# Performance work log

Hardware: AMD Instinct MI355X
Metric: run time of the kernel (lower is better)

## Reference

```python
import jax, jax.numpy as jnp
import numpy as np

N, P, D = 262144, 128, 64
EPS = 1e-5
NEG = -1e30


def setup_inputs() -> dict:
    key = jax.random.key(0)
    ks = jax.random.split(key, 12)
    feature = jax.random.normal(ks[0], (N, D), jnp.float32)
    feature_geo = jax.random.normal(ks[1], (N, D), jnp.float32)
    xyz = jax.random.uniform(ks[2], (N, 3), jnp.float32)
    centers = jax.random.uniform(ks[3], (3,), jnp.float32)
    plane_center = jax.random.uniform(ks[4], (P, 3), jnp.float32)
    nrm = jax.random.normal(ks[5], (P, 3), jnp.float32)
    plane_normal = nrm / jnp.linalg.norm(nrm, axis=1, keepdims=True)
    lo = 0.3 * jax.random.uniform(ks[6], (P, 3), jnp.float32)
    hi = 0.5 + 0.5 * jax.random.uniform(ks[7], (P, 3), jnp.float32)
    # exactly two active axes per plane (one axis of the aabb is zeroed)
    ax = jnp.arange(P) % 3
    keep = (jnp.arange(3)[None, :] != ax[:, None]).astype(jnp.float32)
    plane_xyz_min = lo * keep
    plane_xyz_max = hi * keep
    w1 = 0.05 * jax.random.normal(ks[8], (2 * D, D), jnp.float32)
    b1 = jnp.zeros((D,), jnp.float32)
    w2 = 0.05 * jax.random.normal(ks[9], (D, D), jnp.float32)
    b2 = jnp.zeros((D,), jnp.float32)
    w3 = 0.05 * jax.random.normal(ks[10], (D, 1), jnp.float32)
    b3 = jnp.zeros((1,), jnp.float32)
    g1 = jnp.ones((D,), jnp.float32); be1 = jnp.zeros((D,), jnp.float32)
    m1 = jnp.zeros((D,), jnp.float32); v1 = jnp.ones((D,), jnp.float32)
    g2 = jnp.ones((D,), jnp.float32); be2 = jnp.zeros((D,), jnp.float32)
    m2 = jnp.zeros((D,), jnp.float32); v2 = jnp.ones((D,), jnp.float32)
    return dict(feature=feature, feature_geo=feature_geo, xyz=xyz, centers=centers,
                plane_center=plane_center, plane_normal=plane_normal,
                plane_xyz_min=plane_xyz_min, plane_xyz_max=plane_xyz_max,
                w1=w1, b1=b1, g1=g1, be1=be1, m1=m1, v1=v1,
                w2=w2, b2=b2, g2=g2, be2=be2, m2=m2, v2=v2,
                w3=w3, b3=b3)


def _bn(x, g, b, m, v):
    return (x - m) * (g * jax.lax.rsqrt(v + EPS)) + b


def reference(feature, feature_geo, xyz, centers, plane_center, plane_normal,
              plane_xyz_min, plane_xyz_max, w1, b1, g1, be1, m1, v1,
              w2, b2, g2, be2, m2, v2, w3, b3):
    clouds = xyz + centers                                   # [N,3]
    f = jnp.concatenate([feature, feature_geo], axis=1)      # [N,2D]
    # 1x1 conv MLP == per-point matmul (fc1 -> fc2 with BN+ReLU, fc3)
    h1 = jax.nn.relu(_bn(f @ w1 + b1, g1, be1, m1, v1))      # [N,D]
    h2 = jax.nn.relu(_bn(h1 @ w2 + b2, g2, be2, m2, v2))     # [N,D]
    scores = jax.nn.relu(h2 @ w3 + b3)[:, 0]                 # [N]
    # per-plane aabb mask over the two active axes (xyz_max != 0)
    active = plane_xyz_max != 0                              # [P,3]
    in_rng = (clouds[None] >= plane_xyz_min[:, None]) & (clouds[None] < plane_xyz_max[:, None])
    range_mask = jnp.all(in_rng | ~active[:, None, :], axis=-1)   # [P,N]
    # point-to-plane distance: |(clouds - center) . normal|
    dots = clouds @ plane_normal.T                           # [N,P]
    offs = jnp.sum(plane_center * plane_normal, axis=1)      # [P]
    dist = jnp.abs(dots - offs[None, :]).T                   # [P,N]
    mask = range_mask & (dist < 0.1)                         # [P,N]
    sig = jax.nn.sigmoid(scores)                             # [N]
    on_mask = mask & (sig > 0.5)[None, :]
    off_mask = mask & (sig <= 0.5)[None, :]

    def pool(m):  # masked max-pool of fc2 features over points of one plane
        val = jnp.max(jnp.where(m[:, None], h2, NEG), axis=0)     # [D]
        return jnp.where(jnp.any(m), val, 0.0)

    on_feat = jax.lax.map(pool, on_mask)                     # [P,D]
    off_feat = jax.lax.map(pool, off_mask)                   # [P,D]
    scores_masked = jnp.where(mask, scores[None, :], 0.0)    # [P,N]
    return scores_masked, mask, on_mask, off_mask, on_feat, off_feat
```

## Files before the change

### kernel.cpp

```cpp
#include <hip/hip_runtime.h>
#include <hip/hip_bf16.h>
#include <math.h>

#define NPTS 262144
#define NP   128
#define DD   64
#define NWORDS (NPTS / 64)

__global__ __launch_bounds__(256) void mlp1_kernel(
    const float* __restrict__ feature, const float* __restrict__ feature_geo,
    const float* __restrict__ w1, const float* __restrict__ b1,
    const float* __restrict__ g1, const float* __restrict__ be1,
    const float* __restrict__ m1, const float* __restrict__ v1,
    float* __restrict__ h1_out)
{
    const int n = blockIdx.x * 256 + threadIdx.x;
    float acc[DD];
#pragma unroll
    for (int j = 0; j < DD; ++j) acc[j] = 0.0f;

    const float4* fA = reinterpret_cast<const float4*>(feature) + (size_t)n * 16;
#pragma unroll 1
    for (int q = 0; q < 16; ++q) {
        const float4 fv = fA[q];
        const float* wr = w1 + q * 4 * DD;
#pragma unroll
        for (int j = 0; j < DD; ++j) acc[j] = fmaf(fv.x, wr[j], acc[j]);
#pragma unroll
        for (int j = 0; j < DD; ++j) acc[j] = fmaf(fv.y, wr[DD + j], acc[j]);
#pragma unroll
        for (int j = 0; j < DD; ++j) acc[j] = fmaf(fv.z, wr[2 * DD + j], acc[j]);
#pragma unroll
        for (int j = 0; j < DD; ++j) acc[j] = fmaf(fv.w, wr[3 * DD + j], acc[j]);
    }
    const float4* fB = reinterpret_cast<const float4*>(feature_geo) + (size_t)n * 16;
    const float* w1b = w1 + DD * DD;
#pragma unroll 1
    for (int q = 0; q < 16; ++q) {
        const float4 fv = fB[q];
        const float* wr = w1b + q * 4 * DD;
#pragma unroll
        for (int j = 0; j < DD; ++j) acc[j] = fmaf(fv.x, wr[j], acc[j]);
#pragma unroll
        for (int j = 0; j < DD; ++j) acc[j] = fmaf(fv.y, wr[DD + j], acc[j]);
#pragma unroll
        for (int j = 0; j < DD; ++j) acc[j] = fmaf(fv.z, wr[2 * DD + j], acc[j]);
#pragma unroll
        for (int j = 0; j < DD; ++j) acc[j] = fmaf(fv.w, wr[3 * DD + j], acc[j]);
    }
#pragma unroll
    for (int j = 0; j < DD; ++j) {
        float sc = g1[j] * (1.0f / sqrtf(v1[j] + 1e-5f));
        float h  = fmaf(acc[j] + b1[j] - m1[j], sc, be1[j]);
        acc[j] = fmaxf(h, 0.0f);
    }
    float4* o = reinterpret_cast<float4*>(h1_out) + (size_t)n * 16;
#pragma unroll
    for (int q = 0; q < 16; ++q)
        o[q] = make_float4(acc[4*q+0], acc[4*q+1], acc[4*q+2], acc[4*q+3]);
}

__global__ __launch_bounds__(256) void mlp2_kernel(
    const float* __restrict__ h1_in,
    const float* __restrict__ w2, const float* __restrict__ b2,
    const float* __restrict__ g2, const float* __restrict__ be2,
    const float* __restrict__ m2, const float* __restrict__ v2,
    const float* __restrict__ w3, const float* __restrict__ b3,
    float* __restrict__ h2_out, float* __restrict__ scores_out)
{
    const int n = blockIdx.x * 256 + threadIdx.x;
    float acc[DD];
#pragma unroll
    for (int j = 0; j < DD; ++j) acc[j] = 0.0f;

    const float4* fA = reinterpret_cast<const float4*>(h1_in) + (size_t)n * 16;
#pragma unroll 1
    for (int q = 0; q < 16; ++q) {
        const float4 fv = fA[q];
        const float* wr = w2 + q * 4 * DD;
#pragma unroll
        for (int j = 0; j < DD; ++j) acc[j] = fmaf(fv.x, wr[j], acc[j]);
#pragma unroll
        for (int j = 0; j < DD; ++j) acc[j] = fmaf(fv.y, wr[DD + j], acc[j]);
#pragma unroll
        for (int j = 0; j < DD; ++j) acc[j] = fmaf(fv.z, wr[2 * DD + j], acc[j]);
#pragma unroll
        for (int j = 0; j < DD; ++j) acc[j] = fmaf(fv.w, wr[3 * DD + j], acc[j]);
    }
    float s = 0.0f;
#pragma unroll
    for (int j = 0; j < DD; ++j) {
        float sc = g2[j] * (1.0f / sqrtf(v2[j] + 1e-5f));
        float h  = fmaf(acc[j] + b2[j] - m2[j], sc, be2[j]);
        h = fmaxf(h, 0.0f);
        acc[j] = h;
        s = fmaf(h, w3[j], s);
    }
    s += b3[0];
    float4* o = reinterpret_cast<float4*>(h2_out) + (size_t)n * 16;
#pragma unroll
    for (int q = 0; q < 16; ++q)
        o[q] = make_float4(acc[4*q+0], acc[4*q+1], acc[4*q+2], acc[4*q+3]);
    scores_out[n] = fmaxf(s, 0.0f);
}

__global__ __launch_bounds__(256) void mask_kernel(
    const float* __restrict__ xyz, const float* __restrict__ centers,
    const float* __restrict__ plane_center, const float* __restrict__ plane_normal,
    const float* __restrict__ pmin, const float* __restrict__ pmax,
    const float* __restrict__ scores,
    float* __restrict__ out_sm, float* __restrict__ out_mask,
    float* __restrict__ out_on, float* __restrict__ out_off,
    unsigned long long* __restrict__ hitOn, unsigned long long* __restrict__ hitOff)
{
    __shared__ float4 pl[NP][3];
    const int t = threadIdx.x;
    if (t < NP) {
        float n0 = plane_normal[t*3+0], n1 = plane_normal[t*3+1], n2 = plane_normal[t*3+2];
        float c0 = plane_center[t*3+0], c1 = plane_center[t*3+1], c2 = plane_center[t*3+2];
        float off = (c0*n0 + c1*n1) + c2*n2;
        pl[t][0] = make_float4(n0, n1, n2, off);
        pl[t][1] = make_float4(pmin[t*3+0], pmin[t*3+1], pmin[t*3+2], 0.0f);
        pl[t][2] = make_float4(pmax[t*3+0], pmax[t*3+1], pmax[t*3+2], 0.0f);
    }
    __syncthreads();

    const int n = blockIdx.x * 256 + t;
    const float c0 = xyz[n*3+0] + centers[0];
    const float c1 = xyz[n*3+1] + centers[1];
    const float c2 = xyz[n*3+2] + centers[2];
    const float s  = scores[n];
    const bool on  = (0.5f + 0.5f * tanhf(0.5f * s)) > 0.5f;
    const int lane = t & 63;
    const int word = n >> 6;

    for (int p = 0; p < NP; ++p) {
        float4 nrm = pl[p][0];
        float4 mn  = pl[p][1];
        float4 mx  = pl[p][2];
        float d = fabsf(fmaf(c2, nrm.z, fmaf(c1, nrm.y, c0 * nrm.x)) - nrm.w);
        bool ok0 = (mx.x == 0.0f) | ((c0 >= mn.x) & (c0 < mx.x));
        bool ok1 = (mx.y == 0.0f) | ((c1 >= mn.y) & (c1 < mx.y));
        bool ok2 = (mx.z == 0.0f) | ((c2 >= mn.z) & (c2 < mx.z));
        bool mk  = ok0 & ok1 & ok2 & (d < 0.1f);
        size_t idx = (size_t)p * NPTS + n;
        out_sm[idx]   = mk ? s : 0.0f;
        out_mask[idx] = mk ? 1.0f : 0.0f;
        bool mon  = mk & on;
        bool moff = mk & (!on);
        out_on[idx]  = mon  ? 1.0f : 0.0f;
        out_off[idx] = moff ? 1.0f : 0.0f;
        unsigned long long bOn  = __ballot(mon);
        unsigned long long bOff = __ballot(moff);
        if (lane == 0) {
            hitOn [(size_t)p * NWORDS + word] = bOn;
            hitOff[(size_t)p * NWORDS + word] = bOff;
        }
    }
}

__global__ __launch_bounds__(256) void pool_kernel(
    const float* __restrict__ h2,
    const unsigned long long* __restrict__ hitOn,
    const unsigned long long* __restrict__ hitOff,
    float* __restrict__ partials)
{
    __shared__ float tile[128 * DD];
    __shared__ unsigned long long bm[2][NP][2];
    const int t = threadIdx.x;
    const int lane = t & 63;
    const int wv = t >> 6;

    float accOn[32], accOff[32];
#pragma unroll
    for (int i = 0; i < 32; ++i) { accOn[i] = 0.0f; accOff[i] = 0.0f; }

    for (int cc = 0; cc < 4; ++cc) {
        const int chunk = blockIdx.x * 4 + cc;
        const int base  = chunk * 128;
        const float4* src = reinterpret_cast<const float4*>(h2 + (size_t)base * DD);
        float4* dst = reinterpret_cast<float4*>(tile);
#pragma unroll
        for (int q = 0; q < 8; ++q) dst[t + q * 256] = src[t + q * 256];
        {
            const int p = t & 127;
            const int half = t >> 7;
            const unsigned long long* hsrc = half ? hitOff : hitOn;
            const int w0 = chunk * 2;
            bm[half][p][0] = hsrc[(size_t)p * NWORDS + w0 + 0];
            bm[half][p][1] = hsrc[(size_t)p * NWORDS + w0 + 1];
        }
        __syncthreads();

#pragma unroll
        for (int i = 0; i < 32; ++i) {
            const int p = wv * 32 + i;
            unsigned long long m;
            m = bm[0][p][0];
            while (m) { int nn = __builtin_ctzll(m); m &= m - 1;
                        accOn[i]  = fmaxf(accOn[i],  tile[nn * DD + lane]); }
            m = bm[0][p][1];
            while (m) { int nn = __builtin_ctzll(m); m &= m - 1;
                        accOn[i]  = fmaxf(accOn[i],  tile[(64 + nn) * DD + lane]); }
            m = bm[1][p][0];
            while (m) { int nn = __builtin_ctzll(m); m &= m - 1;
                        accOff[i] = fmaxf(accOff[i], tile[nn * DD + lane]); }
            m = bm[1][p][1];
            while (m) { int nn = __builtin_ctzll(m); m &= m - 1;
                        accOff[i] = fmaxf(accOff[i], tile[(64 + nn) * DD + lane]); }
        }
        __syncthreads();
    }
    const size_t bbase = (size_t)blockIdx.x * NP * 2 * DD;
#pragma unroll
    for (int i = 0; i < 32; ++i) {
        const int p = wv * 32 + i;
        partials[bbase + ((size_t)p * 2 + 0) * DD + lane] = accOn[i];
        partials[bbase + ((size_t)p * 2 + 1) * DD + lane] = accOff[i];
    }
}

__global__ __launch_bounds__(256) void reduce_kernel(
    const float* __restrict__ partials, float* __restrict__ out_feats)
{
    const int u = blockIdx.x * 256 + threadIdx.x;
    float a0 = 0.0f, a1 = 0.0f, a2 = 0.0f, a3 = 0.0f;
    for (int b = 0; b < 512; b += 4) {
        a0 = fmaxf(a0, partials[(size_t)(b + 0) * 16384 + u]);
        a1 = fmaxf(a1, partials[(size_t)(b + 1) * 16384 + u]);
        a2 = fmaxf(a2, partials[(size_t)(b + 2) * 16384 + u]);
        a3 = fmaxf(a3, partials[(size_t)(b + 3) * 16384 + u]);
    }
    const float acc = fmaxf(fmaxf(a0, a1), fmaxf(a2, a3));
    const int p = u >> 7, oo = (u >> 6) & 1, d = u & 63;
    out_feats[oo * (NP * DD) + p * DD + d] = acc;
}

extern "C" void kernel_launch(void* const* d_in, const int* in_sizes, int n_in,
                              void* d_out, int out_size, void* d_ws, size_t ws_size,
                              hipStream_t stream) {
    const float* feature      = (const float*)d_in[0];
    const float* feature_geo  = (const float*)d_in[1];
    const float* xyz          = (const float*)d_in[2];
    const float* centers      = (const float*)d_in[3];
    const float* plane_center = (const float*)d_in[4];
    const float* plane_normal = (const float*)d_in[5];
    const float* pmin         = (const float*)d_in[6];
    const float* pmax         = (const float*)d_in[7];
    const float* w1 = (const float*)d_in[8];
    const float* b1 = (const float*)d_in[9];
    const float* g1 = (const float*)d_in[10];
    const float* be1 = (const float*)d_in[11];
    const float* m1 = (const float*)d_in[12];
    const float* v1 = (const float*)d_in[13];
    const float* w2 = (const float*)d_in[14];
    const float* b2 = (const float*)d_in[15];
    const float* g2 = (const float*)d_in[16];
    const float* be2 = (const float*)d_in[17];
    const float* m2 = (const float*)d_in[18];
    const float* v2 = (const float*)d_in[19];
    const float* w3 = (const float*)d_in[20];
    const float* b3 = (const float*)d_in[21];

    float* out = (float*)d_out;
    const size_t PN = (size_t)NP * NPTS;
    float* out_sm    = out;
    float* out_mask  = out + PN;
    float* out_on    = out + 2 * PN;
    float* out_off   = out + 3 * PN;
    float* out_feats = out + 4 * PN;

    float* h1     = (float*)d_ws;
    float* h2     = h1 + (size_t)NPTS * DD;
    float* scores = h2 + (size_t)NPTS * DD;
    unsigned long long* hitOn  = (unsigned long long*)(scores + NPTS);
    unsigned long long* hitOff = hitOn + (size_t)NP * NWORDS;
    float* partials = h1;

    mlp1_kernel<<<NPTS / 256, 256, 0, stream>>>(
        feature, feature_geo, w1, b1, g1, be1, m1, v1, h1);
    mlp2_kernel<<<NPTS / 256, 256, 0, stream>>>(
        h1, w2, b2, g2, be2, m2, v2, w3, b3, h2, scores);
    mask_kernel<<<NPTS / 256, 256, 0, stream>>>(
        xyz, centers, plane_center, plane_normal, pmin, pmax, scores,
        out_sm, out_mask, out_on, out_off, hitOn, hitOff);
    pool_kernel<<<512, 256, 0, stream>>>(h2, hitOn, hitOff, partials);
    reduce_kernel<<<16384 / 256, 256, 0, stream>>>(partials, out_feats);
}
```

Measured before the change: 892.6 us.

## Replace partials reduction with atomicMax and precompute plane params in prep kernel

The per-block partials buffer and the separate reduce kernel are dropped. Each pool block now merges its nonzero results into the zero-initialised output with integer atomicMax on the float bits, which is valid because the values are non-negative after ReLU. A small prep kernel zeroes the output and packs the plane parameters once. The mask kernel then reads that packed data straight from global memory instead of rebuilding a shared-memory copy in every block. This removes a large partials write and read plus one launch, at the cost of atomic contention and uncached-in-LDS plane loads inside the mask loop.

```diff
diff --git a/kernel.cpp b/kernel.cpp
--- a/kernel.cpp
+++ b/kernel.cpp
@@ -6,6 +6,24 @@
 #define NP   128
 #define DD   64
 #define NWORDS (NPTS / 64)
+
+__global__ __launch_bounds__(256) void prep_kernel(
+    const float* __restrict__ plane_center, const float* __restrict__ plane_normal,
+    const float* __restrict__ pmin, const float* __restrict__ pmax,
+    float* __restrict__ packed, float* __restrict__ out_feats)
+{
+    const int t = threadIdx.x;
+    out_feats[blockIdx.x * 256 + t] = 0.0f;
+    if (blockIdx.x == 0 && t < NP) {
+        float n0 = plane_normal[t*3+0], n1 = plane_normal[t*3+1], n2 = plane_normal[t*3+2];
+        float c0 = plane_center[t*3+0], c1 = plane_center[t*3+1], c2 = plane_center[t*3+2];
+        float off = (c0*n0 + c1*n1) + c2*n2;
+        float4* pp = reinterpret_cast<float4*>(packed) + t * 3;
+        pp[0] = make_float4(n0, n1, n2, off);
+        pp[1] = make_float4(pmin[t*3+0], pmin[t*3+1], pmin[t*3+2], 0.0f);
+        pp[2] = make_float4(pmax[t*3+0], pmax[t*3+1], pmax[t*3+2], 0.0f);
+    }
+}
 
 __global__ __launch_bounds__(256) void mlp1_kernel(
     const float* __restrict__ feature, const float* __restrict__ feature_geo,
@@ -106,25 +124,13 @@
 
 __global__ __launch_bounds__(256) void mask_kernel(
     const float* __restrict__ xyz, const float* __restrict__ centers,
-    const float* __restrict__ plane_center, const float* __restrict__ plane_normal,
-    const float* __restrict__ pmin, const float* __restrict__ pmax,
+    const float* __restrict__ packed,
     const float* __restrict__ scores,
     float* __restrict__ out_sm, float* __restrict__ out_mask,
     float* __restrict__ out_on, float* __restrict__ out_off,
     unsigned long long* __restrict__ hitOn, unsigned long long* __restrict__ hitOff)
 {
-    __shared__ float4 pl[NP][3];
     const int t = threadIdx.x;
-    if (t < NP) {
-        float n0 = plane_normal[t*3+0], n1 = plane_normal[t*3+1], n2 = plane_normal[t*3+2];
-        float c0 = plane_center[t*3+0], c1 = plane_center[t*3+1], c2 = plane_center[t*3+2];
-        float off = (c0*n0 + c1*n1) + c2*n2;
-        pl[t][0] = make_float4(n0, n1, n2, off);
-        pl[t][1] = make_float4(pmin[t*3+0], pmin[t*3+1], pmin[t*3+2], 0.0f);
-        pl[t][2] = make_float4(pmax[t*3+0], pmax[t*3+1], pmax[t*3+2], 0.0f);
-    }
-    __syncthreads();
-
     const int n = blockIdx.x * 256 + t;
     const float c0 = xyz[n*3+0] + centers[0];
     const float c1 = xyz[n*3+1] + centers[1];
@@ -134,10 +140,12 @@
     const int lane = t & 63;
     const int word = n >> 6;
 
+    const float4* pp = reinterpret_cast<const float4*>(packed);
+#pragma unroll 1
     for (int p = 0; p < NP; ++p) {
-        float4 nrm = pl[p][0];
-        float4 mn  = pl[p][1];
-        float4 mx  = pl[p][2];
+        float4 nrm = pp[p*3+0];
+        float4 mn  = pp[p*3+1];
+        float4 mx  = pp[p*3+2];
         float d = fabsf(fmaf(c2, nrm.z, fmaf(c1, nrm.y, c0 * nrm.x)) - nrm.w);
         bool ok0 = (mx.x == 0.0f) | ((c0 >= mn.x) & (c0 < mx.x));
         bool ok1 = (mx.y == 0.0f) | ((c1 >= mn.y) & (c1 < mx.y));
@@ -163,7 +171,7 @@
     const float* __restrict__ h2,
     const unsigned long long* __restrict__ hitOn,
     const unsigned long long* __restrict__ hitOff,
-    float* __restrict__ partials)
+    int* __restrict__ out_feats_i)
 {
     __shared__ float tile[128 * DD];
     __shared__ unsigned long long bm[2][NP][2];
@@ -211,29 +219,12 @@
         }
         __syncthreads();
     }
-    const size_t bbase = (size_t)blockIdx.x * NP * 2 * DD;
 #pragma unroll
     for (int i = 0; i < 32; ++i) {
         const int p = wv * 32 + i;
-        partials[bbase + ((size_t)p * 2 + 0) * DD + lane] = accOn[i];
-        partials[bbase + ((size_t)p * 2 + 1) * DD + lane] = accOff[i];
-    }
-}
-
-__global__ __launch_bounds__(256) void reduce_kernel(
-    const float* __restrict__ partials, float* __restrict__ out_feats)
-{
-    const int u = blockIdx.x * 256 + threadIdx.x;
-    float a0 = 0.0f, a1 = 0.0f, a2 = 0.0f, a3 = 0.0f;
-    for (int b = 0; b < 512; b += 4) {
-        a0 = fmaxf(a0, partials[(size_t)(b + 0) * 16384 + u]);
-        a1 = fmaxf(a1, partials[(size_t)(b + 1) * 16384 + u]);
-        a2 = fmaxf(a2, partials[(size_t)(b + 2) * 16384 + u]);
-        a3 = fmaxf(a3, partials[(size_t)(b + 3) * 16384 + u]);
-    }
-    const float acc = fmaxf(fmaxf(a0, a1), fmaxf(a2, a3));
-    const int p = u >> 7, oo = (u >> 6) & 1, d = u & 63;
-    out_feats[oo * (NP * DD) + p * DD + d] = acc;
+        if (accOn[i]  != 0.0f) atomicMax(&out_feats_i[p * DD + lane],            __float_as_int(accOn[i]));
+        if (accOff[i] != 0.0f) atomicMax(&out_feats_i[NP * DD + p * DD + lane],  __float_as_int(accOff[i]));
+    }
 }
 
 extern "C" void kernel_launch(void* const* d_in, const int* in_sizes, int n_in,
@@ -275,15 +266,16 @@
     float* scores = h2 + (size_t)NPTS * DD;
     unsigned long long* hitOn  = (unsigned long long*)(scores + NPTS);
     unsigned long long* hitOff = hitOn + (size_t)NP * NWORDS;
-    float* partials = h1;
-
+    float* packed = (float*)(hitOff + (size_t)NP * NWORDS);
+
+    prep_kernel<<<64, 256, 0, stream>>>(
+        plane_center, plane_normal, pmin, pmax, packed, out_feats);
     mlp1_kernel<<<NPTS / 256, 256, 0, stream>>>(
         feature, feature_geo, w1, b1, g1, be1, m1, v1, h1);
     mlp2_kernel<<<NPTS / 256, 256, 0, stream>>>(
         h1, w2, b2, g2, be2, m2, v2, w3, b3, h2, scores);
     mask_kernel<<<NPTS / 256, 256, 0, stream>>>(
-        xyz, centers, plane_center, plane_normal, pmin, pmax, scores,
+        xyz, centers, packed, scores,
         out_sm, out_mask, out_on, out_off, hitOn, hitOff);
-    pool_kernel<<<512, 256, 0, stream>>>(h2, hitOn, hitOff, partials);
-    reduce_kernel<<<16384 / 256, 256, 0, stream>>>(partials, out_feats);
-}
+    pool_kernel<<<512, 256, 0, stream>>>(h2, hitOn, hitOff, (int*)out_feats);
+}
```

After: 869.4 us. 1.03x faster.
